# Optimization experiments

Hardware: AMD Instinct MI355X
Metric: run time of the kernel (lower is better)

Reference implementation:

```python
import jax, jax.numpy as jnp
import numpy as np

B, S, D, H = 64, 256, 1024, 1024
F0, F1 = 1024, 1024
STDV = 1.0 / np.sqrt(H)


def setup_inputs() -> dict:
    key = jax.random.key(0)
    ks = jax.random.split(key, 14)
    u = lambda k, shape: jax.random.uniform(k, shape, jnp.float32, -STDV, STDV)
    return {
        "input_feats": jax.random.normal(ks[0], (B, S, D), jnp.float32),
        "feat0": jax.random.normal(ks[1], (B, S, F0), jnp.float32),
        "feat1": jax.random.normal(ks[2], (B, S, F1), jnp.float32),
        "weight_ih": u(ks[3], (3 * H, D)),
        "weight_hh": u(ks[4], (3 * H, H)),
        "weight_fh0": u(ks[5], (2 * H, F0)),
        "weight_fh1": u(ks[6], (2 * H, F1)),
        "bias_ih": u(ks[7], (3 * H,)),
        "bias_hh": u(ks[8], (3 * H,)),
        "bias_fh0": u(ks[9], (2 * H,)),
        "bias_fh1": u(ks[10], (2 * H,)),
    }


def reference(input_feats, feat0, feat1, weight_ih, weight_hh, weight_fh0,
              weight_fh1, bias_ih, bias_hh, bias_fh0, bias_fh1):
    hid = weight_hh.shape[1]
    # Input-to-gate and feature-to-gate projections have no recurrence:
    # batch them over all timesteps up front (same math as per-step F.linear).
    gi = input_feats @ weight_ih.T + bias_ih                      # [B,S,3H]
    gf = (feat0 @ weight_fh0.T + feat1 @ weight_fh1.T
          + bias_fh0 + bias_fh1)                                  # [B,S,2H]
    gi_t = jnp.swapaxes(gi, 0, 1)                                 # [S,B,3H]
    gf_t = jnp.swapaxes(gf, 0, 1)                                 # [S,B,2H]

    def step(hx, xs):
        gi_s, gf_s = xs
        gh = hx @ weight_hh.T + bias_hh                           # [B,3H]
        i_r, i_i, i_n = jnp.split(gi_s, 3, axis=1)
        h_r, h_i, h_n = jnp.split(gh, 3, axis=1)
        f_r, f_i = jnp.split(gf_s, 2, axis=1)
        resetgate = jax.nn.sigmoid(i_r + h_r + f_r)
        inputgate = jax.nn.sigmoid(i_i + h_i + f_i)
        newgate = jnp.tanh(i_n + resetgate * h_n)
        hy = newgate + inputgate * (hx - newgate)
        return hy, hy

    h0 = jnp.zeros((input_feats.shape[0], hid), input_feats.dtype)
    h_last, ys = jax.lax.scan(step, h0, (gi_t, gf_t))
    output = jnp.swapaxes(ys, 0, 1)                               # [B,S,H]
    return output, h_last
```

## Files before the change

### kernel.cpp

```cpp
#include <hip/hip_runtime.h>

typedef unsigned short u16;
typedef __attribute__((ext_vector_type(8))) short short8;
typedef __attribute__((ext_vector_type(4))) float f32x4;
typedef __attribute__((ext_vector_type(4))) unsigned u32x4;

#define BB 64
#define SS 256
#define HH 1024
#define NG 3072
#define KK 1024
#define NOUT ((size_t)BB * SS * HH)

#define OFF_GSUM 0ull
#define OFF_HB0 100663296ull
#define OFF_HB1 100794368ull
#define OFF_BAR 100925440ull
#define WS_NEED 100925568ull

__device__ __forceinline__ float bf2f_u(unsigned x) {
  unsigned u = x << 16;
  float f;
  __builtin_memcpy(&f, &u, 4);
  return f;
}
__device__ __forceinline__ u16 f2bf(float f) {
  unsigned u;
  __builtin_memcpy(&u, &f, 4);
  u = (u + 0x7fffu + ((u >> 16) & 1u)) >> 16;
  return (u16)u;
}
__device__ __forceinline__ short8 cvt8(f32x4 lo, f32x4 hi) {
  union { unsigned u[4]; short8 s; } r;
  asm("v_cvt_pk_bf16_f32 %0, %1, %2" : "=v"(r.u[0]) : "v"(lo[0]), "v"(lo[1]));
  asm("v_cvt_pk_bf16_f32 %0, %1, %2" : "=v"(r.u[1]) : "v"(lo[2]), "v"(lo[3]));
  asm("v_cvt_pk_bf16_f32 %0, %1, %2" : "=v"(r.u[2]) : "v"(hi[0]), "v"(hi[1]));
  asm("v_cvt_pk_bf16_f32 %0, %1, %2" : "=v"(r.u[3]) : "v"(hi[2]), "v"(hi[3]));
  return r.s;
}
__device__ __forceinline__ float sigmoidf_(float x) {
  return __builtin_amdgcn_rcpf(1.f + __expf(-x));
}
__device__ __forceinline__ float tanhf_(float x) {
  return 2.f * __builtin_amdgcn_rcpf(1.f + __expf(-2.f * x)) - 1.f;
}

typedef const __attribute__((address_space(1))) void* gcptr;
typedef __attribute__((address_space(3))) void* lptr;

__global__ __launch_bounds__(256) void gemm_fused(
    const float* __restrict__ X, const float* __restrict__ F0, const float* __restrict__ F1,
    const float* __restrict__ Wih, const float* __restrict__ Wf0, const float* __restrict__ Wf1,
    const float* __restrict__ bih, const float* __restrict__ bf0, const float* __restrict__ bf1,
    u16* __restrict__ C) {
  __shared__ __align__(16) float ldsA[128 * 32];
  __shared__ __align__(16) float ldsB[128 * 32];
  const int t = threadIdx.x;
  const int nwg = gridDim.x;
  const int cpx = nwg >> 3;
  const int wg = (blockIdx.x & 7) * cpx + (blockIdx.x >> 3);
  const int ntn = NG / 128;
  const int m0 = (wg / ntn) * 128;
  const int n0 = (wg % ntn) * 128;
  const int lane = t & 63, wv = t >> 6;
  const int wm = wv >> 1, wn = wv & 1;

  f32x4 acc[4][4] = {};

  const int nsrc = (n0 < 2048) ? 3 : 1;
  for (int src = 0; src < nsrc; ++src) {
    const float* Ap = (src == 0) ? X : ((src == 1) ? F0 : F1);
    const float* Wp = (src == 0) ? Wih : ((src == 1) ? Wf0 : Wf1);
    const float* Abase = Ap + (size_t)m0 * KK;
    const float* Wbase = Wp + (size_t)n0 * KK;
    for (int k0 = 0; k0 < KK; k0 += 32) {
#pragma unroll
      for (int c = 0; c < 4; ++c) {
        const int idx = c * 256 + t;
        const int row = idx >> 3, q = idx & 7;
        const int qs = q ^ (row & 7);
        __builtin_amdgcn_global_load_lds((gcptr)(Abase + (size_t)row * KK + k0 + qs * 4),
                                         (lptr)(&ldsA[idx * 4]), 16, 0, 0);
        __builtin_amdgcn_global_load_lds((gcptr)(Wbase + (size_t)row * KK + k0 + qs * 4),
                                         (lptr)(&ldsB[idx * 4]), 16, 0, 0);
      }
      __syncthreads();
      short8 af[4], bw[4];
      const int g0 = (lane >> 4) * 2;
#pragma unroll
      for (int i = 0; i < 4; ++i) {
        {
          const int row = wm * 64 + i * 16 + (lane & 15);
          const int ga = g0 ^ (row & 7), gb = (g0 + 1) ^ (row & 7);
          f32x4 lo = *(const f32x4*)&ldsA[row * 32 + ga * 4];
          f32x4 hi = *(const f32x4*)&ldsA[row * 32 + gb * 4];
          af[i] = cvt8(lo, hi);
        }
        {
          const int row = wn * 64 + i * 16 + (lane & 15);
          const int ga = g0 ^ (row & 7), gb = (g0 + 1) ^ (row & 7);
          f32x4 lo = *(const f32x4*)&ldsB[row * 32 + ga * 4];
          f32x4 hi = *(const f32x4*)&ldsB[row * 32 + gb * 4];
          bw[i] = cvt8(lo, hi);
        }
      }
#pragma unroll
      for (int i = 0; i < 4; ++i)
#pragma unroll
        for (int j = 0; j < 4; ++j)
          acc[i][j] = __builtin_amdgcn_mfma_f32_16x16x32_bf16(af[i], bw[j], acc[i][j], 0, 0, 0);
      __syncthreads();
    }
  }
#pragma unroll
  for (int j = 0; j < 4; ++j) {
    const int col = n0 + wn * 64 + j * 16 + (lane & 15);
    float bias = bih[col];
    if (col < 2048) bias += bf0[col] + bf1[col];
#pragma unroll
    for (int i = 0; i < 4; ++i) {
      const int row = m0 + wm * 64 + i * 16 + (lane >> 4) * 4;
#pragma unroll
      for (int r = 0; r < 4; ++r)
        C[(size_t)(row + r) * NG + col] = f2bf(acc[i][j][r] + bias);
    }
  }
}

#define SB0() __builtin_amdgcn_sched_barrier(0)

#define ISSUE8(buf, bkk)                                                        \
  _Pragma("unroll")                                                             \
  for (int i_ = 0; i_ < 8; ++i_)                                                \
    asm volatile("global_load_dwordx4 %0, %1, off sc0 sc1"                      \
                 : "=v"(buf[i_]) : "v"(ap + ((bkk) + i_) * 32));

#define CONSUME8(buf, bkk)                                                      \
  _Pragma("unroll")                                                             \
  for (int i_ = 0; i_ < 8; ++i_) {                                              \
    const int ko_ = ((bkk) + i_) * 64 + kb;                                     \
    short8 br_ = *(const short8*)(s0 + (ko_ ^ sw));                             \
    short8 bj_ = *(const short8*)(s1 + (ko_ ^ sw));                             \
    short8 bn_ = *(const short8*)(s2 + (ko_ ^ sw));                             \
    ar = __builtin_amdgcn_mfma_f32_16x16x32_bf16(buf[i_], br_, ar, 0, 0, 0);    \
    ai = __builtin_amdgcn_mfma_f32_16x16x32_bf16(buf[i_], bj_, ai, 0, 0, 0);    \
    an = __builtin_amdgcn_mfma_f32_16x16x32_bf16(buf[i_], bn_, an, 0, 0, 0);    \
  }

#define ISSUE_GSUM(snext)                                                       \
  _Pragma("unroll")                                                             \
  for (int r_ = 0; r_ < 4; ++r_) {                                              \
    const u16* gp_ = gsum + ((size_t)(mb + quad * 4 + r_) * 256 + (size_t)(snext)) * 3072 + jl; \
    asm volatile("global_load_ushort %0, %1, off" : "=v"(pgu[r_ * 3 + 0]) : "v"(gp_));          \
    asm volatile("global_load_ushort %0, %1, off" : "=v"(pgu[r_ * 3 + 1]) : "v"(gp_ + 1024));   \
    asm volatile("global_load_ushort %0, %1, off" : "=v"(pgu[r_ * 3 + 2]) : "v"(gp_ + 2048));   \
  }

__global__ __launch_bounds__(256, 1) void scan_kernel(
    const u16* __restrict__ gsum, const float* __restrict__ Whh, const float* __restrict__ bhh,
    u16* __restrict__ h0buf, u16* __restrict__ h1buf,
    float* __restrict__ out, unsigned* __restrict__ bar) {
  extern __shared__ u16 wlds[];
  const int t = threadIdx.x, w = blockIdx.x;
  const int j0 = w * 16;
  for (int c = t; c < 48 * 128; c += 256) {
    int q = c >> 7, chunk = c & 127;
    int g = q >> 4, i = q & 15;
    const float* wf = Whh + ((size_t)(g * 1024 + j0 + i)) * 1024 + chunk * 8;
    short8 v = cvt8(*(const f32x4*)wf, *(const f32x4*)(wf + 4));
    *(short8*)((char*)wlds + q * 2048 + ((chunk * 16) ^ (i << 4))) = v;
  }
  const int lane = t & 63;
  const int bi = lane & 15;
  const int quad = lane >> 4;
  const int jl = j0 + bi;
  const int mb = (t >> 6) * 16;
  const float bhr = bhh[jl];
  const float bhi = bhh[1024 + jl];
  const float bhn = bhh[2048 + jl];
  __syncthreads();

  float hreg[4] = {0.f, 0.f, 0.f, 0.f};

  const int kb = quad * 16;
  const int sw = bi << 4;
  const char* wbytes = (const char*)wlds;
  const char* s0 = wbytes + (size_t)(0 + bi) * 2048;
  const char* s1 = wbytes + (size_t)(16 + bi) * 2048;
  const char* s2 = wbytes + (size_t)(32 + bi) * 2048;

  unsigned* myctr = bar + (w & 7);

  unsigned pgu[12];
  ISSUE_GSUM(0);
  asm volatile("s_waitcnt vmcnt(0)" ::: "memory");
  SB0();

  short8 aA[8], aB[8], aC[8], aD[8];
  for (int s = 0; s < 256; ++s) {
    f32x4 ar = {0.f, 0.f, 0.f, 0.f};
    f32x4 ai = {0.f, 0.f, 0.f, 0.f};
    f32x4 an = {0.f, 0.f, 0.f, 0.f};
    if (s > 0) {
      asm volatile("s_waitcnt vmcnt(24)" ::: "memory");
      SB0();
      CONSUME8(aA, 0);
      asm volatile("s_waitcnt vmcnt(16)" ::: "memory");
      SB0();
      CONSUME8(aB, 8);
      asm volatile("s_waitcnt vmcnt(8)" ::: "memory");
      SB0();
      CONSUME8(aC, 16);
      asm volatile("s_waitcnt vmcnt(0)" ::: "memory");
      SB0();
      CONSUME8(aD, 24);
      SB0();
    }
    u16* hw = (s & 1) ? h0buf : h1buf;
    float hy4[4];
    unsigned hv4[4];
#pragma unroll
    for (int r = 0; r < 4; ++r) {
      float rg = sigmoidf_(bf2f_u(pgu[r * 3 + 0]) + ar[r] + bhr);
      float ig = sigmoidf_(bf2f_u(pgu[r * 3 + 1]) + ai[r] + bhi);
      float ng = tanhf_(bf2f_u(pgu[r * 3 + 2]) + rg * (an[r] + bhn));
      float hy = ng + ig * (hreg[r] - ng);
      hreg[r] = hy;
      hy4[r] = hy;
      hv4[r] = (unsigned)f2bf(hy);
    }
    if (s < 255) {
#pragma unroll
      for (int r = 0; r < 4; ++r) {
        int b = mb + quad * 4 + r;
        asm volatile("global_store_short %0, %1, off sc0 sc1"
                     :: "v"(hw + (size_t)b * 1024 + jl), "v"(hv4[r]) : "memory");
      }
    }
#pragma unroll
    for (int r = 0; r < 4; ++r) {
      int b = mb + quad * 4 + r;
      size_t m = (size_t)b * 256 + s;
      asm volatile("global_store_dword %0, %1, off nt"
                   :: "v"(out + m * 1024 + jl), "v"(hy4[r]) : "memory");
    }
    if (s < 255) {
      ISSUE_GSUM(s + 1);
      asm volatile("s_waitcnt vmcnt(16)" ::: "memory");
      SB0();
      __builtin_amdgcn_s_barrier();
      if (t == 0) {
        unsigned one = 1;
        asm volatile("global_atomic_add %0, %1, off" :: "v"(myctr), "v"(one) : "memory");
        const unsigned target = 64u * (unsigned)(s + 1);
        for (;;) {
          u32x4 va, vb;
          asm volatile("global_load_dwordx4 %0, %2, off sc0 sc1\n\t"
                       "global_load_dwordx4 %1, %3, off sc0 sc1\n\t"
                       "s_waitcnt vmcnt(0)"
                       : "=v"(va), "=v"(vb) : "v"(bar), "v"(bar + 4) : "memory");
          unsigned sum = va[0] + va[1] + va[2] + va[3] + vb[0] + vb[1] + vb[2] + vb[3];
          if (sum >= target) break;
          __builtin_amdgcn_s_sleep(1);
        }
      }
      __builtin_amdgcn_s_barrier();
      SB0();
      const u16* hcur = (s & 1) ? h0buf : h1buf;
      const u16* ap = hcur + (size_t)(mb + bi) * 1024 + quad * 8;
      ISSUE8(aA, 0);
      ISSUE8(aB, 8);
      ISSUE8(aC, 16);
      ISSUE8(aD, 24);
      SB0();
    }
  }
#pragma unroll
  for (int r = 0; r < 4; ++r) {
    int b = mb + quad * 4 + r;
    out[NOUT + (size_t)b * 1024 + jl] = hreg[r];
  }
}

extern "C" void kernel_launch(void* const* d_in, const int* in_sizes, int n_in,
                              void* d_out, int out_size, void* d_ws, size_t ws_size,
                              hipStream_t stream) {
  if (ws_size < WS_NEED) return;
  const float* x   = (const float*)d_in[0];
  const float* f0  = (const float*)d_in[1];
  const float* f1  = (const float*)d_in[2];
  const float* wih = (const float*)d_in[3];
  const float* whh = (const float*)d_in[4];
  const float* wf0 = (const float*)d_in[5];
  const float* wf1 = (const float*)d_in[6];
  const float* bih = (const float*)d_in[7];
  const float* bhh = (const float*)d_in[8];
  const float* bf0 = (const float*)d_in[9];
  const float* bf1 = (const float*)d_in[10];

  char* ws = (char*)d_ws;
  u16* gsum = (u16*)(ws + OFF_GSUM);
  u16* hb0 = (u16*)(ws + OFF_HB0);
  u16* hb1 = (u16*)(ws + OFF_HB1);
  unsigned* bar = (unsigned*)(ws + OFF_BAR);

  hipMemsetAsync(bar, 0, 128, stream);
  hipMemsetAsync(hb0, 0, 131072, stream);
  hipMemsetAsync(hb1, 0, 131072, stream);

  gemm_fused<<<dim3(3072), dim3(256), 0, stream>>>(x, f0, f1, wih, wf0, wf1, bih, bf0, bf1, gsum);

  hipFuncSetAttribute(reinterpret_cast<const void*>(&scan_kernel),
                      hipFuncAttributeMaxDynamicSharedMemorySize, 98304);
  scan_kernel<<<dim3(64), dim3(256), 98304, stream>>>(gsum, whh, bhh, hb0, hb1, (float*)d_out, bar);
}
```

Measured before the change: 2.234 ms.

## Split recurrent K-reduction across two wave halves with LDS partial-sum exchange

The scan kernel now launches 512 threads per block instead of 256. Each pair of waves splits the 1024-long hidden-state reduction in half, so each wave issues 16 h-loads instead of 32 and does half the MFMAs per step. The partial accumulators are exchanged through an extra 24KB of LDS with an added block barrier, and each wave then finishes the gate math for 2 of the 4 rows. This is meant to shorten the per-step serial latency of the recurrence, at the cost of an extra LDS round trip and barrier each step.

```diff
diff --git a/kernel.cpp b/kernel.cpp
--- a/kernel.cpp
+++ b/kernel.cpp
@@ -128,42 +128,43 @@
 }
 
 #define SB0() __builtin_amdgcn_sched_barrier(0)
-
-#define ISSUE8(buf, bkk)                                                        \
+#define LDSW 98304
+
+#define ISSUE16()                                                               \
   _Pragma("unroll")                                                             \
-  for (int i_ = 0; i_ < 8; ++i_)                                                \
+  for (int i_ = 0; i_ < 16; ++i_)                                               \
     asm volatile("global_load_dwordx4 %0, %1, off sc0 sc1"                      \
-                 : "=v"(buf[i_]) : "v"(ap + ((bkk) + i_) * 32));
-
-#define CONSUME8(buf, bkk)                                                      \
+                 : "=v"(hbuf[i_]) : "v"(ap + i_ * 32));
+
+#define CONSUME8(bkk)                                                           \
   _Pragma("unroll")                                                             \
-  for (int i_ = 0; i_ < 8; ++i_) {                                              \
-    const int ko_ = ((bkk) + i_) * 64 + kb;                                     \
+  for (int i_ = (bkk); i_ < (bkk) + 8; ++i_) {                                  \
+    const int ko_ = (half * 16 + i_) * 64 + kb;                                 \
     short8 br_ = *(const short8*)(s0 + (ko_ ^ sw));                             \
     short8 bj_ = *(const short8*)(s1 + (ko_ ^ sw));                             \
     short8 bn_ = *(const short8*)(s2 + (ko_ ^ sw));                             \
-    ar = __builtin_amdgcn_mfma_f32_16x16x32_bf16(buf[i_], br_, ar, 0, 0, 0);    \
-    ai = __builtin_amdgcn_mfma_f32_16x16x32_bf16(buf[i_], bj_, ai, 0, 0, 0);    \
-    an = __builtin_amdgcn_mfma_f32_16x16x32_bf16(buf[i_], bn_, an, 0, 0, 0);    \
+    ar = __builtin_amdgcn_mfma_f32_16x16x32_bf16(hbuf[i_], br_, ar, 0, 0, 0);   \
+    ai = __builtin_amdgcn_mfma_f32_16x16x32_bf16(hbuf[i_], bj_, ai, 0, 0, 0);   \
+    an = __builtin_amdgcn_mfma_f32_16x16x32_bf16(hbuf[i_], bn_, an, 0, 0, 0);   \
   }
 
 #define ISSUE_GSUM(snext)                                                       \
   _Pragma("unroll")                                                             \
-  for (int r_ = 0; r_ < 4; ++r_) {                                              \
-    const u16* gp_ = gsum + ((size_t)(mb + quad * 4 + r_) * 256 + (size_t)(snext)) * 3072 + jl; \
-    asm volatile("global_load_ushort %0, %1, off" : "=v"(pgu[r_ * 3 + 0]) : "v"(gp_));          \
-    asm volatile("global_load_ushort %0, %1, off" : "=v"(pgu[r_ * 3 + 1]) : "v"(gp_ + 1024));   \
-    asm volatile("global_load_ushort %0, %1, off" : "=v"(pgu[r_ * 3 + 2]) : "v"(gp_ + 2048));   \
-  }
-
-__global__ __launch_bounds__(256, 1) void scan_kernel(
+  for (int rr_ = 0; rr_ < 2; ++rr_) {                                           \
+    const u16* gp_ = gsum + ((size_t)(mb + quad * 4 + rbase + rr_) * 256 + (size_t)(snext)) * 3072 + jl; \
+    asm volatile("global_load_ushort %0, %1, off" : "=v"(pgu[rr_ * 3 + 0]) : "v"(gp_));          \
+    asm volatile("global_load_ushort %0, %1, off" : "=v"(pgu[rr_ * 3 + 1]) : "v"(gp_ + 1024));   \
+    asm volatile("global_load_ushort %0, %1, off" : "=v"(pgu[rr_ * 3 + 2]) : "v"(gp_ + 2048));   \
+  }
+
+__global__ __launch_bounds__(512, 1) void scan_kernel(
     const u16* __restrict__ gsum, const float* __restrict__ Whh, const float* __restrict__ bhh,
     u16* __restrict__ h0buf, u16* __restrict__ h1buf,
     float* __restrict__ out, unsigned* __restrict__ bar) {
   extern __shared__ u16 wlds[];
   const int t = threadIdx.x, w = blockIdx.x;
   const int j0 = w * 16;
-  for (int c = t; c < 48 * 128; c += 256) {
+  for (int c = t; c < 48 * 128; c += 512) {
     int q = c >> 7, chunk = c & 127;
     int g = q >> 4, i = q & 15;
     const float* wf = Whh + ((size_t)(g * 1024 + j0 + i)) * 1024 + chunk * 8;
@@ -171,16 +172,20 @@
     *(short8*)((char*)wlds + q * 2048 + ((chunk * 16) ^ (i << 4))) = v;
   }
   const int lane = t & 63;
+  const int wv = t >> 6;
+  const int half = wv >> 2;
+  const int wq = wv & 3;
   const int bi = lane & 15;
   const int quad = lane >> 4;
   const int jl = j0 + bi;
-  const int mb = (t >> 6) * 16;
+  const int mb = wq * 16;
+  const int rbase = half * 2;
   const float bhr = bhh[jl];
   const float bhi = bhh[1024 + jl];
   const float bhn = bhh[2048 + jl];
   __syncthreads();
 
-  float hreg[4] = {0.f, 0.f, 0.f, 0.f};
+  float hreg[2] = {0.f, 0.f};
 
   const int kb = quad * 16;
   const int sw = bi << 4;
@@ -188,65 +193,72 @@
   const char* s0 = wbytes + (size_t)(0 + bi) * 2048;
   const char* s1 = wbytes + (size_t)(16 + bi) * 2048;
   const char* s2 = wbytes + (size_t)(32 + bi) * 2048;
+  char* pbase = (char*)wlds + LDSW;
+  const int pw = wv ^ 4;
 
   unsigned* myctr = bar + (w & 7);
 
-  unsigned pgu[12];
+  unsigned pgu[6];
   ISSUE_GSUM(0);
   asm volatile("s_waitcnt vmcnt(0)" ::: "memory");
   SB0();
 
-  short8 aA[8], aB[8], aC[8], aD[8];
+  short8 hbuf[16];
   for (int s = 0; s < 256; ++s) {
     f32x4 ar = {0.f, 0.f, 0.f, 0.f};
     f32x4 ai = {0.f, 0.f, 0.f, 0.f};
     f32x4 an = {0.f, 0.f, 0.f, 0.f};
     if (s > 0) {
-      asm volatile("s_waitcnt vmcnt(24)" ::: "memory");
-      SB0();
-      CONSUME8(aA, 0);
-      asm volatile("s_waitcnt vmcnt(16)" ::: "memory");
-      SB0();
-      CONSUME8(aB, 8);
       asm volatile("s_waitcnt vmcnt(8)" ::: "memory");
       SB0();
-      CONSUME8(aC, 16);
+      CONSUME8(0);
       asm volatile("s_waitcnt vmcnt(0)" ::: "memory");
       SB0();
-      CONSUME8(aD, 24);
-      SB0();
-    }
+      CONSUME8(8);
+      SB0();
+    }
+    *(f32x4*)(pbase + ((0 * 8 + wv) * 64 + lane) * 16) = ar;
+    *(f32x4*)(pbase + ((1 * 8 + wv) * 64 + lane) * 16) = ai;
+    *(f32x4*)(pbase + ((2 * 8 + wv) * 64 + lane) * 16) = an;
+    asm volatile("s_waitcnt lgkmcnt(0)" ::: "memory");
+    SB0();
+    __builtin_amdgcn_s_barrier();
+    SB0();
+    ar += *(const f32x4*)(pbase + ((0 * 8 + pw) * 64 + lane) * 16);
+    ai += *(const f32x4*)(pbase + ((1 * 8 + pw) * 64 + lane) * 16);
+    an += *(const f32x4*)(pbase + ((2 * 8 + pw) * 64 + lane) * 16);
     u16* hw = (s & 1) ? h0buf : h1buf;
-    float hy4[4];
-    unsigned hv4[4];
-#pragma unroll
-    for (int r = 0; r < 4; ++r) {
-      float rg = sigmoidf_(bf2f_u(pgu[r * 3 + 0]) + ar[r] + bhr);
-      float ig = sigmoidf_(bf2f_u(pgu[r * 3 + 1]) + ai[r] + bhi);
-      float ng = tanhf_(bf2f_u(pgu[r * 3 + 2]) + rg * (an[r] + bhn));
-      float hy = ng + ig * (hreg[r] - ng);
-      hreg[r] = hy;
-      hy4[r] = hy;
-      hv4[r] = (unsigned)f2bf(hy);
+    float hy2[2];
+    unsigned hv2[2];
+#pragma unroll
+    for (int rr = 0; rr < 2; ++rr) {
+      const int r = rbase + rr;
+      float rg = sigmoidf_(bf2f_u(pgu[rr * 3 + 0]) + ar[r] + bhr);
+      float ig = sigmoidf_(bf2f_u(pgu[rr * 3 + 1]) + ai[r] + bhi);
+      float ng = tanhf_(bf2f_u(pgu[rr * 3 + 2]) + rg * (an[r] + bhn));
+      float hy = ng + ig * (hreg[rr] - ng);
+      hreg[rr] = hy;
+      hy2[rr] = hy;
+      hv2[rr] = (unsigned)f2bf(hy);
     }
     if (s < 255) {
 #pragma unroll
-      for (int r = 0; r < 4; ++r) {
-        int b = mb + quad * 4 + r;
+      for (int rr = 0; rr < 2; ++rr) {
+        int b = mb + quad * 4 + rbase + rr;
         asm volatile("global_store_short %0, %1, off sc0 sc1"
-                     :: "v"(hw + (size_t)b * 1024 + jl), "v"(hv4[r]) : "memory");
+                     :: "v"(hw + (size_t)b * 1024 + jl), "v"(hv2[rr]) : "memory");
       }
     }
 #pragma unroll
-    for (int r = 0; r < 4; ++r) {
-      int b = mb + quad * 4 + r;
+    for (int rr = 0; rr < 2; ++rr) {
+      int b = mb + quad * 4 + rbase + rr;
       size_t m = (size_t)b * 256 + s;
       asm volatile("global_store_dword %0, %1, off nt"
-                   :: "v"(out + m * 1024 + jl), "v"(hy4[r]) : "memory");
+                   :: "v"(out + m * 1024 + jl), "v"(hy2[rr]) : "memory");
     }
     if (s < 255) {
       ISSUE_GSUM(s + 1);
-      asm volatile("s_waitcnt vmcnt(16)" ::: "memory");
+      asm volatile("s_waitcnt vmcnt(8)" ::: "memory");
       SB0();
       __builtin_amdgcn_s_barrier();
       if (t == 0) {
@@ -267,18 +279,15 @@
       __builtin_amdgcn_s_barrier();
       SB0();
       const u16* hcur = (s & 1) ? h0buf : h1buf;
-      const u16* ap = hcur + (size_t)(mb + bi) * 1024 + quad * 8;
-      ISSUE8(aA, 0);
-      ISSUE8(aB, 8);
-      ISSUE8(aC, 16);
-      ISSUE8(aD, 24);
-      SB0();
-    }
-  }
-#pragma unroll
-  for (int r = 0; r < 4; ++r) {
-    int b = mb + quad * 4 + r;
-    out[NOUT + (size_t)b * 1024 + jl] = hreg[r];
+      const u16* ap = hcur + (size_t)(mb + bi) * 1024 + half * 512 + quad * 8;
+      ISSUE16();
+      SB0();
+    }
+  }
+#pragma unroll
+  for (int rr = 0; rr < 2; ++rr) {
+    int b = mb + quad * 4 + rbase + rr;
+    out[NOUT + (size_t)b * 1024 + jl] = hreg[rr];
   }
 }
 
@@ -311,6 +320,6 @@
   gemm_fused<<<dim3(3072), dim3(256), 0, stream>>>(x, f0, f1, wih, wf0, wf1, bih, bf0, bf1, gsum);
 
   hipFuncSetAttribute(reinterpret_cast<const void*>(&scan_kernel),
-                      hipFuncAttributeMaxDynamicSharedMemorySize, 98304);
-  scan_kernel<<<dim3(64), dim3(256), 98304, stream>>>(gsum, whh, bhh, hb0, hb1, (float*)d_out, bar);
-}
+                      hipFuncAttributeMaxDynamicSharedMemorySize, 122880);
+  scan_kernel<<<dim3(64), dim3(512), 122880, stream>>>(gsum, whh, bhh, hb0, hb1, (float*)d_out, bar);
+}
```

New measurement: 2.376 ms. +6.3%, slower.
